# Optimization experiments

Hardware: AMD Instinct MI355X
Metric: run time of the kernel (lower is better)

## Reference

```python
import jax, jax.numpy as jnp
import numpy as np

B, S, R, H, NH, HD = 32, 1026, 256, 1024, 16, 64

def setup_inputs() -> dict:
    key = jax.random.key(0)
    ks = jax.random.split(key, 8)
    sc = 0.02
    return {
        "q_low": jax.random.normal(ks[0], (B, S, R), jnp.float32),
        "k_low": jax.random.normal(ks[1], (B, S, R), jnp.float32),
        "v_low": jax.random.normal(ks[2], (B, S, R), jnp.float32),
        "Wq": jax.random.normal(ks[3], (R, H), jnp.float32) * sc,
        "bq": jnp.zeros((H,), jnp.float32),
        "Wk": jax.random.normal(ks[4], (R, H), jnp.float32) * sc,
        "bk": jnp.zeros((H,), jnp.float32),
        "Wv": jax.random.normal(ks[5], (R, H), jnp.float32) * sc,
        "bv": jnp.zeros((H,), jnp.float32),
        "Wo_down": jax.random.normal(ks[6], (H, R), jnp.float32) * sc,
    }

def reference(q_low, k_low, v_low, Wq, bq, Wk, bk, Wv, bv, Wo_down):
    # Up-project low-rank activations to full Q, K, V: [B,S,R] @ [R,H] -> [B,S,H]
    q = q_low @ Wq + bq
    k = k_low @ Wk + bk
    v = v_low @ Wv + bv
    # split heads: [B,S,NH,HD] -> [B,NH,S,HD]
    def split(x):
        return x.reshape(B, S, NH, HD).transpose(0, 2, 1, 3)
    qh, kh, vh = split(q), split(k), split(v)
    scores = jnp.einsum('bhqd,bhkd->bhqk', qh, kh) / jnp.sqrt(jnp.float32(HD))
    probs = jax.nn.softmax(scores, axis=-1)  # dropout p=0
    ctx = jnp.einsum('bhqk,bhkd->bhqd', probs, vh)
    ctx = ctx.transpose(0, 2, 1, 3).reshape(B, S, H)
    # Down-project with low-rank activation (gelu)
    out_low = jax.nn.gelu(ctx @ Wo_down, approximate=False)
    return out_low
```

## Files before the change

kernel.cpp:

```cpp
#include <hip/hip_runtime.h>
#include <hip/hip_bf16.h>
#include <math.h>

using short8   = __attribute__((ext_vector_type(8))) short;
using floatx4  = __attribute__((ext_vector_type(4))) float;
using floatx16 = __attribute__((ext_vector_type(16))) float;

#define B_N  32
#define S_N  1026
#define R_N  256
#define H_N  1024
#define NH_N 16
#define HD_N 64
#define SP_N 1088
#define KTILES 17
#define CS_LD 136

__device__ __forceinline__ float bf2f(__hip_bfloat16 x) { return __bfloat162float(x); }
__device__ __forceinline__ __hip_bfloat16 f2bf(float x) { return __float2bfloat16(x); }

__device__ __forceinline__ float fast_exp2(float x) {
#if __has_builtin(__builtin_amdgcn_exp2f)
    return __builtin_amdgcn_exp2f(x);
#else
    return exp2f(x);
#endif
}

__device__ __forceinline__ unsigned cvtpk(float lo, float hi_) {
    unsigned r;
    asm("v_cvt_pk_bf16_f32 %0, %1, %2" : "=v"(r) : "v"(lo), "v"(hi_));
    return r;
}

__device__ __forceinline__ void gl_lds16(const void* g, void* l) {
    __builtin_amdgcn_global_load_lds(
        (const __attribute__((address_space(1))) unsigned int*)g,
        (__attribute__((address_space(3))) unsigned int*)l, 16, 0, 0);
}

__device__ __forceinline__ int xcd_swz(int o, int nwg) {
    return ((nwg & 7) == 0) ? ((o & 7) * (nwg >> 3) + (o >> 3)) : o;
}

__device__ __forceinline__ short8 cvt8(const float* __restrict__ p) {
    floatx4 a = *(const floatx4*)p;
    floatx4 b = *(const floatx4*)(p + 4);
    short8 o;
    __hip_bfloat16* op = (__hip_bfloat16*)&o;
    op[0] = f2bf(a[0]); op[1] = f2bf(a[1]); op[2] = f2bf(a[2]); op[3] = f2bf(a[3]);
    op[4] = f2bf(b[0]); op[5] = f2bf(b[1]); op[6] = f2bf(b[2]); op[7] = f2bf(b[3]);
    return o;
}

__global__ __launch_bounds__(256) void transpose3_kernel(
    const float* __restrict__ a, const float* __restrict__ b, const float* __restrict__ c,
    __hip_bfloat16* __restrict__ oa, __hip_bfloat16* __restrict__ ob,
    __hip_bfloat16* __restrict__ oc, int K, int N) {
    __shared__ __hip_bfloat16 t[32][33];
    const float* in = (blockIdx.z == 0) ? a : (blockIdx.z == 1) ? b : c;
    __hip_bfloat16* out = (blockIdx.z == 0) ? oa : (blockIdx.z == 1) ? ob : oc;
    const int k0 = blockIdx.x * 32, n0 = blockIdx.y * 32;
    const int tx = threadIdx.x & 31, ty = threadIdx.x >> 5;
#pragma unroll
    for (int j = 0; j < 32; j += 8)
        t[ty + j][tx] = f2bf(in[(size_t)(k0 + ty + j) * N + n0 + tx]);
    __syncthreads();
#pragma unroll
    for (int j = 0; j < 32; j += 8)
        out[(size_t)(n0 + ty + j) * K + k0 + tx] = t[tx][ty + j];
}

__global__ __launch_bounds__(256) void transpose_kernel(const float* __restrict__ in,
                                                        __hip_bfloat16* __restrict__ out,
                                                        int K, int N) {
    __shared__ __hip_bfloat16 t[32][33];
    const int k0 = blockIdx.x * 32, n0 = blockIdx.y * 32;
    const int tx = threadIdx.x & 31, ty = threadIdx.x >> 5;
#pragma unroll
    for (int j = 0; j < 32; j += 8)
        t[ty + j][tx] = f2bf(in[(size_t)(k0 + ty + j) * N + n0 + tx]);
    __syncthreads();
#pragma unroll
    for (int j = 0; j < 32; j += 8)
        out[(size_t)(n0 + ty + j) * K + k0 + tx] = t[tx][ty + j];
}

__global__ __launch_bounds__(256) void cvtx_kernel(
    const float* __restrict__ q, const float* __restrict__ k, const float* __restrict__ v,
    __hip_bfloat16* __restrict__ oq, __hip_bfloat16* __restrict__ ok,
    __hip_bfloat16* __restrict__ ov, int n8) {
    int idx = blockIdx.x * 256 + threadIdx.x;
    if (idx >= n8) return;
    const float* s = (blockIdx.y == 0) ? q : (blockIdx.y == 1) ? k : v;
    __hip_bfloat16* d = (blockIdx.y == 0) ? oq : (blockIdx.y == 1) ? ok : ov;
    *(short8*)(d + (size_t)idx * 8) = cvt8(s + (size_t)idx * 8);
}

__global__ void padv_kernel(__hip_bfloat16* __restrict__ Vt, int total) {
    int idx = blockIdx.x * 256 + threadIdx.x;
    if (idx < total) {
        int p  = idx % (SP_N - S_N);
        int rd = idx / (SP_N - S_N);
        Vt[(size_t)rd * SP_N + S_N + p] = f2bf(0.f);
    }
}

__global__ __launch_bounds__(256) void qkvproj_kernel(
    const __hip_bfloat16* __restrict__ Xq, const __hip_bfloat16* __restrict__ Xk,
    const __hip_bfloat16* __restrict__ Xv,
    const __hip_bfloat16* __restrict__ WqT, const __hip_bfloat16* __restrict__ WkT,
    const __hip_bfloat16* __restrict__ WvT,
    const float* __restrict__ bq, const float* __restrict__ bk,
    const float* __restrict__ bv,
    __hip_bfloat16* __restrict__ Qc, __hip_bfloat16* __restrict__ Kc,
    __hip_bfloat16* __restrict__ Vc, int Mc, float qscale) {
    __shared__ char smem[65536];
    typedef __hip_bfloat16 (*AB_t)[128][64];
    AB_t As = (AB_t)smem;
    AB_t Bs = (AB_t)(smem + 32768);
    __hip_bfloat16* Cs = (__hip_bfloat16*)smem;

    const int nx = gridDim.x;
    const int nwg = nx * 8 * 3;
    const int o = blockIdx.x + nx * (blockIdx.y + 8 * blockIdx.z);
    const int tlin = xcd_swz(o, nwg);
    const int ty = tlin & 7;
    const int rest = tlin >> 3;
    const int tx = rest % nx, tz = rest / nx;

    const __hip_bfloat16* X  = (tz == 0) ? Xq  : (tz == 1) ? Xk  : Xv;
    const __hip_bfloat16* WT = (tz == 0) ? WqT : (tz == 1) ? WkT : WvT;
    const float* bias        = (tz == 0) ? bq  : (tz == 1) ? bk  : bv;
    __hip_bfloat16* out      = (tz == 0) ? Qc  : (tz == 1) ? Kc  : Vc;
    const float oscale = (tz == 0) ? qscale : 1.0f;
    const int mode = (tz == 2);

    const int tid  = threadIdx.x;
    const int wave = tid >> 6, lane = tid & 63;
    const int quad = lane >> 4, l16 = lane & 15;
    const int tm = tx * 128, tn = ty * 128;
    const int mw = (wave >> 1) * 64, nw = (wave & 1) * 64;
    const int lr = lane >> 3;
    const int sc = (lane & 7) ^ lr;

    floatx4 acc[4][4] = {};

    auto stage = [&](int bb, int kk) {
#pragma unroll
        for (int s8 = 0; s8 < 4; ++s8) {
            int row = wave * 32 + s8 * 8;
            int gm = tm + row + lr; if (gm >= Mc) gm = Mc - 1;
            gl_lds16(X + (size_t)gm * R_N + kk + sc * 8, &As[bb][row][0]);
            gl_lds16(WT + (size_t)(tn + row + lr) * R_N + kk + sc * 8, &Bs[bb][row][0]);
        }
    };

    stage(0, 0);
    __syncthreads();

    for (int t = 0; t < R_N / 64; ++t) {
        const int bb = t & 1;
        if (t + 1 < R_N / 64) stage(bb ^ 1, (t + 1) * 64);
        short8 af[4][2], bfr[4][2];
#pragma unroll
        for (int mb = 0; mb < 4; ++mb) {
            int row = mw + mb * 16 + l16;
            const char* rp = (const char*)&As[bb][row][0];
#pragma unroll
            for (int k2 = 0; k2 < 2; ++k2)
                af[mb][k2] = *(const short8*)(rp + ((((k2 * 4 + quad)) ^ (row & 7)) << 4));
        }
#pragma unroll
        for (int nb = 0; nb < 4; ++nb) {
            int row = nw + nb * 16 + l16;
            const char* rp = (const char*)&Bs[bb][row][0];
#pragma unroll
            for (int k2 = 0; k2 < 2; ++k2)
                bfr[nb][k2] = *(const short8*)(rp + ((((k2 * 4 + quad)) ^ (row & 7)) << 4));
        }
        if (mode == 0) {
#pragma unroll
            for (int mb = 0; mb < 4; ++mb)
#pragma unroll
                for (int nb = 0; nb < 4; ++nb) {
                    acc[mb][nb] = __builtin_amdgcn_mfma_f32_16x16x32_bf16(af[mb][0], bfr[nb][0], acc[mb][nb], 0, 0, 0);
                    acc[mb][nb] = __builtin_amdgcn_mfma_f32_16x16x32_bf16(af[mb][1], bfr[nb][1], acc[mb][nb], 0, 0, 0);
                }
        } else {
#pragma unroll
            for (int mb = 0; mb < 4; ++mb)
#pragma unroll
                for (int nb = 0; nb < 4; ++nb) {
                    acc[mb][nb] = __builtin_amdgcn_mfma_f32_16x16x32_bf16(bfr[nb][0], af[mb][0], acc[mb][nb], 0, 0, 0);
                    acc[mb][nb] = __builtin_amdgcn_mfma_f32_16x16x32_bf16(bfr[nb][1], af[mb][1], acc[mb][nb], 0, 0, 0);
                }
        }
        __syncthreads();
    }

    if (mode == 0) {
#pragma unroll
        for (int mb = 0; mb < 4; ++mb)
#pragma unroll
            for (int nb = 0; nb < 4; ++nb) {
                int j = nw + nb * 16 + l16;
                float bv_ = bias[tn + j];
#pragma unroll
                for (int r = 0; r < 4; ++r) {
                    int i = mw + mb * 16 + quad * 4 + r;
                    Cs[i * CS_LD + j] = f2bf(oscale * (acc[mb][nb][r] + bv_));
                }
            }
    } else {
#pragma unroll
        for (int mb = 0; mb < 4; ++mb)
#pragma unroll
            for (int nb = 0; nb < 4; ++nb)
#pragma unroll
                for (int r = 0; r < 4; ++r) {
                    int i = nw + nb * 16 + quad * 4 + r;
                    int j = mw + mb * 16 + l16;
                    Cs[i * CS_LD + j] = f2bf(acc[mb][nb][r] + bias[tn + i]);
                }
    }
    __syncthreads();

    const int i = tid >> 1, half = tid & 1;
    if (mode == 0) {
        int m = tm + i;
        if (m < Mc) {
            int bl = m / S_N, s = m - bl * S_N;
            int h = (tn >> 6) + half;
            size_t ob = ((size_t)((bl * NH_N + h) * S_N + s)) * HD_N;
            const __hip_bfloat16* src = Cs + i * CS_LD + half * 64;
#pragma unroll
            for (int j = 0; j < 8; ++j)
                *(short8*)(out + ob + j * 8) = *(const short8*)(src + j * 8);
        }
    } else {
        int n = tn + i;
        int h = n >> 6, d = n & 63;
        const __hip_bfloat16* src = Cs + i * CS_LD + half * 64;
#pragma unroll
        for (int j = 0; j < 8; ++j) {
            int m0 = tm + half * 64 + j * 8;
            if (m0 >= Mc) continue;
            short8 w = *(const short8*)(src + j * 8);
            int bl = m0 / S_N, s0 = m0 - bl * S_N;
            size_t ob = ((size_t)((bl * NH_N + h) * HD_N + d)) * SP_N;
            if (s0 + 8 <= S_N) {
                const unsigned* wp = (const unsigned*)&w;
#pragma unroll
                for (int k = 0; k < 4; ++k)
                    *(unsigned*)(out + ob + s0 + 2 * k) = wp[k];
            } else {
                const __hip_bfloat16* we = (const __hip_bfloat16*)&w;
#pragma unroll
                for (int e = 0; e < 8; ++e) {
                    int m = m0 + e;
                    int bl2 = m / S_N, s2 = m - bl2 * S_N;
                    out[((size_t)((bl2 * NH_N + h) * HD_N + d)) * SP_N + s2] = we[e];
                }
            }
        }
    }
}

__global__ __launch_bounds__(256, 3) void attn_kernel(
    const __hip_bfloat16* __restrict__ Qh,
    const __hip_bfloat16* __restrict__ Kh,
    const __hip_bfloat16* __restrict__ Vt,
    __hip_bfloat16* __restrict__ ctx) {
    __shared__ __hip_bfloat16 Kl[2][64][64];
    __shared__ __hip_bfloat16 Vl[2][64][64];

    const int ny = gridDim.y;
    const int nwg = gridDim.x * ny;
    const int o = blockIdx.x + gridDim.x * blockIdx.y;
    const int tlin = xcd_swz(o, nwg);
    const int bh = tlin / ny;
    const int q0 = (tlin % ny) * 128;

    const int tid = threadIdx.x;
    const int wave = tid >> 6, lane = tid & 63;
    const int c = lane & 31, hi = lane >> 5, c7 = c & 7;
    const size_t base  = (size_t)bh * S_N * HD_N;
    const size_t vbase = (size_t)bh * HD_N * SP_N;

    const int lr = lane >> 3;
    const int sc = (lane & 7) ^ lr;

    short8 qf[4];
    {
        int qrow = q0 + wave * 32 + c;
        if (qrow > S_N - 1) qrow = S_N - 1;
        const __hip_bfloat16* qp = Qh + base + (size_t)qrow * HD_N + hi * 8;
#pragma unroll
        for (int i = 0; i < 4; ++i) qf[i] = *(const short8*)(qp + 16 * i);
    }

    floatx16 oacc[2] = {};
    float lsum = 0.f;

    auto stage = [&](int bb, int kt) {
#pragma unroll
        for (int j = 0; j < 2; ++j) {
            int r = 16 * wave + 8 * j + lr;
            int krow = kt + r;
            if (krow > S_N - 1) krow = S_N - 1;
            gl_lds16(Kh + base + (size_t)krow * HD_N + sc * 8,
                     &Kl[bb][16 * wave + 8 * j][0]);
            gl_lds16(Vt + vbase + (size_t)r * SP_N + kt + sc * 8,
                     &Vl[bb][16 * wave + 8 * j][0]);
        }
    };

    stage(0, 0);
    __syncthreads();

    int bb = 0;
    for (int t = 0; t < KTILES; ++t) {
        const int kt = t * 64;
        if (t + 1 < KTILES) stage(bb ^ 1, kt + 64);
        const bool last = (kt + 64 > S_N);

        short8 pa[2][2];
#pragma unroll
        for (int sub = 0; sub < 2; ++sub) {
            floatx16 sacc = {};
            __builtin_amdgcn_s_setprio(1);
#pragma unroll
            for (int i = 0; i < 4; ++i) {
                short8 kf = *(const short8*)&Kl[bb][32 * sub + c][(((2 * i + hi) ^ c7) << 3)];
                sacc = __builtin_amdgcn_mfma_f32_32x32x16_bf16(kf, qf[i], sacc, 0, 0, 0);
            }
            __builtin_amdgcn_s_setprio(0);
            float ps[16];
            if (!last) {
#pragma unroll
                for (int r = 0; r < 16; ++r) ps[r] = fast_exp2(sacc[r]);
            } else {
#pragma unroll
                for (int r = 0; r < 16; ++r) {
                    int key = kt + 32 * sub + (r & 3) + 8 * (r >> 2) + 4 * hi;
                    ps[r] = (key < S_N) ? fast_exp2(sacc[r]) : 0.f;
                }
            }
#pragma unroll
            for (int r = 0; r < 16; ++r) lsum += ps[r];
#pragma unroll
            for (int step = 0; step < 2; ++step) {
                unsigned w0 = cvtpk(ps[8 * step + 0], ps[8 * step + 1]);
                unsigned w1 = cvtpk(ps[8 * step + 2], ps[8 * step + 3]);
                unsigned w2 = cvtpk(ps[8 * step + 4], ps[8 * step + 5]);
                unsigned w3 = cvtpk(ps[8 * step + 6], ps[8 * step + 7]);
                asm("v_permlane32_swap_b32 %0, %1" : "+v"(w0), "+v"(w2));
                asm("v_permlane32_swap_b32 %0, %1" : "+v"(w1), "+v"(w3));
                union { unsigned u[4]; short8 s; } fu;
                fu.u[0] = w0; fu.u[1] = w1; fu.u[2] = w2; fu.u[3] = w3;
                pa[sub][step] = fu.s;
            }
        }

        __builtin_amdgcn_s_setprio(1);
#pragma unroll
        for (int db = 0; db < 2; ++db)
#pragma unroll
            for (int sub = 0; sub < 2; ++sub)
#pragma unroll
                for (int step = 0; step < 2; ++step) {
                    short8 vf = *(const short8*)
                        &Vl[bb][32 * db + c][((((sub * 2 + step) * 2 + hi) ^ c7) << 3)];
                    oacc[db] = __builtin_amdgcn_mfma_f32_32x32x16_bf16(pa[sub][step], vf, oacc[db], 0, 0, 0);
                }
        __builtin_amdgcn_s_setprio(0);

        __syncthreads();
        bb ^= 1;
    }

    lsum += __shfl_xor(lsum, 32);
    float rs = 1.0f / lsum;

    const int bl = bh / NH_N, h = bh - bl * NH_N;
    const int srow0 = q0 + wave * 32;
#pragma unroll
    for (int r = 0; r < 16; ++r) {
        int q = (r & 3) + 8 * (r >> 2) + 4 * hi;
        float rr = __shfl(rs, q, 32);
        int s = srow0 + q;
        if (s < S_N) {
            size_t o2 = ((size_t)(bl * S_N + s)) * H_N + h * HD_N + c;
            ctx[o2]      = f2bf(oacc[0][r] * rr);
            ctx[o2 + 32] = f2bf(oacc[1][r] * rr);
        }
    }
}

__global__ __launch_bounds__(256) void dproj_kernel(
    const __hip_bfloat16* __restrict__ X,
    const __hip_bfloat16* __restrict__ WT,
    float* __restrict__ out,
    int Mc) {
    __shared__ char smem[49152];
    typedef __hip_bfloat16 (*A_t)[64][64];
    typedef __hip_bfloat16 (*B_t)[128][64];
    A_t As = (A_t)smem;
    B_t Bs = (B_t)(smem + 16384);
    float* Csf = (float*)smem;

    const int tx = blockIdx.x, ty = blockIdx.y;

    const int tid  = threadIdx.x;
    const int wave = tid >> 6, lane = tid & 63;
    const int quad = lane >> 4, l16 = lane & 15;
    const int tm = tx * 64, tn = ty * 128;
    const int mw = (wave >> 1) * 32, nw = (wave & 1) * 64;
    const int lr = lane >> 3;
    const int sc = (lane & 7) ^ lr;

    floatx4 acc[2][4] = {};

    auto stage = [&](int bb, int kk) {
#pragma unroll
        for (int s8 = 0; s8 < 2; ++s8) {
            int row = wave * 16 + s8 * 8;
            int gm = tm + row + lr; if (gm >= Mc) gm = Mc - 1;
            gl_lds16(X + (size_t)gm * H_N + kk + sc * 8, &As[bb][row][0]);
        }
#pragma unroll
        for (int s8 = 0; s8 < 4; ++s8) {
            int row = wave * 32 + s8 * 8;
            gl_lds16(WT + (size_t)(tn + row + lr) * H_N + kk + sc * 8, &Bs[bb][row][0]);
        }
    };

    stage(0, 0);
    __syncthreads();

    for (int t = 0; t < H_N / 64; ++t) {
        const int bb = t & 1;
        if (t + 1 < H_N / 64) stage(bb ^ 1, (t + 1) * 64);
        short8 af[2][2], bfr[4][2];
#pragma unroll
        for (int mb = 0; mb < 2; ++mb) {
            int row = mw + mb * 16 + l16;
            const char* rp = (const char*)&As[bb][row][0];
#pragma unroll
            for (int k2 = 0; k2 < 2; ++k2)
                af[mb][k2] = *(const short8*)(rp + ((((k2 * 4 + quad)) ^ (row & 7)) << 4));
        }
#pragma unroll
        for (int nb = 0; nb < 4; ++nb) {
            int row = nw + nb * 16 + l16;
            const char* rp = (const char*)&Bs[bb][row][0];
#pragma unroll
            for (int k2 = 0; k2 < 2; ++k2)
                bfr[nb][k2] = *(const short8*)(rp + ((((k2 * 4 + quad)) ^ (row & 7)) << 4));
        }
#pragma unroll
        for (int mb = 0; mb < 2; ++mb)
#pragma unroll
            for (int nb = 0; nb < 4; ++nb) {
                acc[mb][nb] = __builtin_amdgcn_mfma_f32_16x16x32_bf16(af[mb][0], bfr[nb][0], acc[mb][nb], 0, 0, 0);
                acc[mb][nb] = __builtin_amdgcn_mfma_f32_16x16x32_bf16(af[mb][1], bfr[nb][1], acc[mb][nb], 0, 0, 0);
            }
        __syncthreads();
    }

#pragma unroll
    for (int mb = 0; mb < 2; ++mb)
#pragma unroll
        for (int nb = 0; nb < 4; ++nb)
#pragma unroll
            for (int r = 0; r < 4; ++r) {
                int i = mw + mb * 16 + quad * 4 + r;
                int j = nw + nb * 16 + l16;
                float x = acc[mb][nb][r];
                Csf[i * CS_LD + j] = 0.5f * x * (1.0f + erff(x * 0.70710678118654752f));
            }
    __syncthreads();

    {
        const int i = tid >> 2, q32 = tid & 3;
        int m = tm + i;
        if (m < Mc) {
            const float* src = Csf + i * CS_LD + q32 * 32;
            float* dst = out + (size_t)m * R_N + tn + q32 * 32;
#pragma unroll
            for (int jj = 0; jj < 8; ++jj)
                *(floatx4*)(dst + jj * 4) = *(const floatx4*)(src + jj * 4);
        }
    }
}

extern "C" void kernel_launch(void* const* d_in, const int* in_sizes, int n_in,
                              void* d_out, int out_size, void* d_ws, size_t ws_size,
                              hipStream_t stream) {
    const float* q_low = (const float*)d_in[0];
    const float* k_low = (const float*)d_in[1];
    const float* v_low = (const float*)d_in[2];
    const float* Wq    = (const float*)d_in[3];
    const float* bq    = (const float*)d_in[4];
    const float* Wk    = (const float*)d_in[5];
    const float* bk    = (const float*)d_in[6];
    const float* Wv    = (const float*)d_in[7];
    const float* bv    = (const float*)d_in[8];
    const float* Wo    = (const float*)d_in[9];
    float* out = (float*)d_out;
    (void)in_sizes; (void)n_in; (void)out_size;

    const float QSCALE = 0.125f * 1.44269504088896f;
    const size_t SZ_W = (size_t)H_N * R_N * 2;

    int C = 32;
    while (C > 1) {
        size_t qk = (size_t)C * NH_N * S_N * HD_N * 2;
        size_t vv = (size_t)C * NH_N * HD_N * SP_N * 2;
        size_t cx = (size_t)C * S_N * H_N * 2;
        if (4 * SZ_W + 2 * qk + vv + cx <= ws_size) break;
        C >>= 1;
    }

    char* ws = (char*)d_ws;
    const size_t SZ_QK = (size_t)C * NH_N * S_N * HD_N * 2;
    const size_t SZ_V  = (size_t)C * NH_N * HD_N * SP_N * 2;
    __hip_bfloat16* WqT = (__hip_bfloat16*)(ws);
    __hip_bfloat16* WkT = (__hip_bfloat16*)(ws + SZ_W);
    __hip_bfloat16* WvT = (__hip_bfloat16*)(ws + 2 * SZ_W);
    __hip_bfloat16* WoT = (__hip_bfloat16*)(ws + 3 * SZ_W);
    __hip_bfloat16* Qc  = (__hip_bfloat16*)(ws + 4 * SZ_W);
    __hip_bfloat16* Kc  = (__hip_bfloat16*)(ws + 4 * SZ_W + SZ_QK);
    __hip_bfloat16* Vc  = (__hip_bfloat16*)(ws + 4 * SZ_W + 2 * SZ_QK);
    __hip_bfloat16* ctc = (__hip_bfloat16*)(ws + 4 * SZ_W + 2 * SZ_QK + SZ_V);

    {
        dim3 tg(R_N / 32, H_N / 32, 3);
        transpose3_kernel<<<tg, 256, 0, stream>>>(Wq, Wk, Wv, WqT, WkT, WvT, R_N, H_N);
        dim3 to(H_N / 32, R_N / 32);
        transpose_kernel<<<to, 256, 0, stream>>>(Wo, WoT, H_N, R_N);
    }

    {
        int total = C * NH_N * HD_N * (SP_N - S_N);
        padv_kernel<<<(total + 255) / 256, 256, 0, stream>>>(Vc, total);
    }

    for (int c0 = 0; c0 < B_N; c0 += C) {
        const int Mc = C * S_N;
        const size_t xoff = (size_t)c0 * S_N * R_N;

        __hip_bfloat16* Xq = ctc;
        __hip_bfloat16* Xk = ctc + (size_t)Mc * R_N;
        __hip_bfloat16* Xv = ctc + 2 * (size_t)Mc * R_N;
        {
            int n8 = Mc * R_N / 8;
            dim3 cg((n8 + 255) / 256, 3);
            cvtx_kernel<<<cg, 256, 0, stream>>>(q_low + xoff, k_low + xoff, v_low + xoff,
                                                Xq, Xk, Xv, n8);
        }

        dim3 pg((Mc + 127) / 128, H_N / 128, 3);
        qkvproj_kernel<<<pg, 256, 0, stream>>>(Xq, Xk, Xv, WqT, WkT, WvT,
                                               bq, bk, bv, Qc, Kc, Vc, Mc, QSCALE);

        dim3 ag(C * NH_N, (S_N + 127) / 128);
        attn_kernel<<<ag, 256, 0, stream>>>(Qc, Kc, Vc, ctc);

        dim3 dg((Mc + 63) / 64, R_N / 128);
        dproj_kernel<<<dg, 256, 0, stream>>>(ctc, WoT, out + xoff, Mc);
    }
}
```

Baseline: 532.9 us.

## Shrink QKV proj K-tile, use MFMA row sums, and XCD-swizzle down-projection grid

Three independent changes. The QKV projection now stages 32-wide K slices instead of 64, with a matching 4-way swizzle, which roughly halves shared memory so more workgroups can reside per CU. The attention kernel now computes softmax row sums with an extra MFMA against a ones vector instead of scalar adds and cross-lane shuffles. The down-projection launches a 1-D grid padded to a multiple of eight and remapped through the XCD swizzle for better L2 locality. The costs are more K-loop iterations and barriers in the projection, and extra MFMA work in attention.

Result: faster. 518.1 us (-2.8%).

```diff
diff --git a/kernel.cpp b/kernel.cpp
--- a/kernel.cpp
+++ b/kernel.cpp
@@ -115,10 +115,10 @@
     const float* __restrict__ bv,
     __hip_bfloat16* __restrict__ Qc, __hip_bfloat16* __restrict__ Kc,
     __hip_bfloat16* __restrict__ Vc, int Mc, float qscale) {
-    __shared__ char smem[65536];
-    typedef __hip_bfloat16 (*AB_t)[128][64];
+    __shared__ char smem[34816];
+    typedef __hip_bfloat16 (*AB_t)[128][32];
     AB_t As = (AB_t)smem;
-    AB_t Bs = (AB_t)(smem + 32768);
+    AB_t Bs = (AB_t)(smem + 16384);
     __hip_bfloat16* Cs = (__hip_bfloat16*)smem;
 
     const int nx = gridDim.x;
@@ -141,60 +141,50 @@
     const int quad = lane >> 4, l16 = lane & 15;
     const int tm = tx * 128, tn = ty * 128;
     const int mw = (wave >> 1) * 64, nw = (wave & 1) * 64;
-    const int lr = lane >> 3;
-    const int sc = (lane & 7) ^ lr;
+    const int lr = lane >> 2;
+    const int sc4 = (lane & 3) ^ (lr & 3);
 
     floatx4 acc[4][4] = {};
 
     auto stage = [&](int bb, int kk) {
 #pragma unroll
-        for (int s8 = 0; s8 < 4; ++s8) {
-            int row = wave * 32 + s8 * 8;
+        for (int s16 = 0; s16 < 2; ++s16) {
+            int row = wave * 32 + s16 * 16;
             int gm = tm + row + lr; if (gm >= Mc) gm = Mc - 1;
-            gl_lds16(X + (size_t)gm * R_N + kk + sc * 8, &As[bb][row][0]);
-            gl_lds16(WT + (size_t)(tn + row + lr) * R_N + kk + sc * 8, &Bs[bb][row][0]);
+            gl_lds16(X + (size_t)gm * R_N + kk + sc4 * 8, &As[bb][row][0]);
+            gl_lds16(WT + (size_t)(tn + row + lr) * R_N + kk + sc4 * 8, &Bs[bb][row][0]);
         }
     };
 
     stage(0, 0);
     __syncthreads();
 
-    for (int t = 0; t < R_N / 64; ++t) {
+    for (int t = 0; t < R_N / 32; ++t) {
         const int bb = t & 1;
-        if (t + 1 < R_N / 64) stage(bb ^ 1, (t + 1) * 64);
-        short8 af[4][2], bfr[4][2];
+        if (t + 1 < R_N / 32) stage(bb ^ 1, (t + 1) * 32);
+        short8 af[4], bfr[4];
 #pragma unroll
         for (int mb = 0; mb < 4; ++mb) {
             int row = mw + mb * 16 + l16;
-            const char* rp = (const char*)&As[bb][row][0];
-#pragma unroll
-            for (int k2 = 0; k2 < 2; ++k2)
-                af[mb][k2] = *(const short8*)(rp + ((((k2 * 4 + quad)) ^ (row & 7)) << 4));
+            af[mb] = *(const short8*)((const char*)&As[bb][row][0] + ((quad ^ (row & 3)) << 4));
         }
 #pragma unroll
         for (int nb = 0; nb < 4; ++nb) {
             int row = nw + nb * 16 + l16;
-            const char* rp = (const char*)&Bs[bb][row][0];
-#pragma unroll
-            for (int k2 = 0; k2 < 2; ++k2)
-                bfr[nb][k2] = *(const short8*)(rp + ((((k2 * 4 + quad)) ^ (row & 7)) << 4));
+            bfr[nb] = *(const short8*)((const char*)&Bs[bb][row][0] + ((quad ^ (row & 3)) << 4));
         }
         if (mode == 0) {
 #pragma unroll
             for (int mb = 0; mb < 4; ++mb)
 #pragma unroll
-                for (int nb = 0; nb < 4; ++nb) {
-                    acc[mb][nb] = __builtin_amdgcn_mfma_f32_16x16x32_bf16(af[mb][0], bfr[nb][0], acc[mb][nb], 0, 0, 0);
-                    acc[mb][nb] = __builtin_amdgcn_mfma_f32_16x16x32_bf16(af[mb][1], bfr[nb][1], acc[mb][nb], 0, 0, 0);
-                }
+                for (int nb = 0; nb < 4; ++nb)
+                    acc[mb][nb] = __builtin_amdgcn_mfma_f32_16x16x32_bf16(af[mb], bfr[nb], acc[mb][nb], 0, 0, 0);
         } else {
 #pragma unroll
             for (int mb = 0; mb < 4; ++mb)
 #pragma unroll
-                for (int nb = 0; nb < 4; ++nb) {
-                    acc[mb][nb] = __builtin_amdgcn_mfma_f32_16x16x32_bf16(bfr[nb][0], af[mb][0], acc[mb][nb], 0, 0, 0);
-                    acc[mb][nb] = __builtin_amdgcn_mfma_f32_16x16x32_bf16(bfr[nb][1], af[mb][1], acc[mb][nb], 0, 0, 0);
-                }
+                for (int nb = 0; nb < 4; ++nb)
+                    acc[mb][nb] = __builtin_amdgcn_mfma_f32_16x16x32_bf16(bfr[nb], af[mb], acc[mb][nb], 0, 0, 0);
         }
         __syncthreads();
     }
@@ -291,6 +281,9 @@
     const int lr = lane >> 3;
     const int sc = (lane & 7) ^ lr;
 
+    const short ONE = 0x3F80;
+    const short8 onesb = {ONE, ONE, ONE, ONE, ONE, ONE, ONE, ONE};
+
     short8 qf[4];
     {
         int qrow = q0 + wave * 32 + c;
@@ -301,7 +294,7 @@
     }
 
     floatx16 oacc[2] = {};
-    float lsum = 0.f;
+    floatx16 rsacc = {};
 
     auto stage = [&](int bb, int kt) {
 #pragma unroll
@@ -347,8 +340,6 @@
                     ps[r] = (key < S_N) ? fast_exp2(sacc[r]) : 0.f;
                 }
             }
-#pragma unroll
-            for (int r = 0; r < 16; ++r) lsum += ps[r];
 #pragma unroll
             for (int step = 0; step < 2; ++step) {
                 unsigned w0 = cvtpk(ps[8 * step + 0], ps[8 * step + 1]);
@@ -374,23 +365,25 @@
                         &Vl[bb][32 * db + c][((((sub * 2 + step) * 2 + hi) ^ c7) << 3)];
                     oacc[db] = __builtin_amdgcn_mfma_f32_32x32x16_bf16(pa[sub][step], vf, oacc[db], 0, 0, 0);
                 }
+#pragma unroll
+        for (int sub = 0; sub < 2; ++sub)
+#pragma unroll
+            for (int step = 0; step < 2; ++step)
+                rsacc = __builtin_amdgcn_mfma_f32_32x32x16_bf16(pa[sub][step], onesb, rsacc, 0, 0, 0);
         __builtin_amdgcn_s_setprio(0);
 
         __syncthreads();
         bb ^= 1;
     }
 
-    lsum += __shfl_xor(lsum, 32);
-    float rs = 1.0f / lsum;
-
     const int bl = bh / NH_N, h = bh - bl * NH_N;
     const int srow0 = q0 + wave * 32;
 #pragma unroll
     for (int r = 0; r < 16; ++r) {
         int q = (r & 3) + 8 * (r >> 2) + 4 * hi;
-        float rr = __shfl(rs, q, 32);
         int s = srow0 + q;
         if (s < S_N) {
+            float rr = 1.0f / rsacc[r];
             size_t o2 = ((size_t)(bl * S_N + s)) * H_N + h * HD_N + c;
             ctx[o2]      = f2bf(oacc[0][r] * rr);
             ctx[o2 + 32] = f2bf(oacc[1][r] * rr);
@@ -410,7 +403,10 @@
     B_t Bs = (B_t)(smem + 16384);
     float* Csf = (float*)smem;
 
-    const int tx = blockIdx.x, ty = blockIdx.y;
+    const int nx = (Mc + 63) >> 6;
+    const int tlin = xcd_swz(blockIdx.x, gridDim.x);
+    if (tlin >= nx * 2) return;
+    const int ty = tlin & 1, tx = tlin >> 1;
 
     const int tid  = threadIdx.x;
     const int wave = tid >> 6, lane = tid & 63;
@@ -568,7 +564,8 @@
         dim3 ag(C * NH_N, (S_N + 127) / 128);
         attn_kernel<<<ag, 256, 0, stream>>>(Qc, Kc, Vc, ctc);
 
-        dim3 dg((Mc + 63) / 64, R_N / 128);
-        dproj_kernel<<<dg, 256, 0, stream>>>(ctc, WoT, out + xoff, Mc);
-    }
-}
+        int nxd = (Mc + 63) / 64;
+        int dg1 = ((nxd * 2 + 7) / 8) * 8;
+        dproj_kernel<<<dg1, 256, 0, stream>>>(ctc, WoT, out + xoff, Mc);
+    }
+}
```
